# Kernel optimization log

Measured on AMD Instinct MI355X. Metric: run time of the kernel, lower is better.

The kernel has to match this reference:

```python
import jax, jax.numpy as jnp
import numpy as np

DIM = 1024
STATE = 256
B, S = 4, 4096

def setup_inputs() -> dict:
    key = jax.random.key(0)
    ks = jax.random.split(key, 8)
    sc_b = 1.0 / np.sqrt(DIM)
    sc_c = 1.0 / np.sqrt(STATE)
    return {
        "x": jax.random.normal(ks[0], (B, S, DIM), dtype=jnp.float32),
        "A": jax.random.normal(ks[1], (STATE,), dtype=jnp.float32) * 0.02,
        "B_w": jax.random.uniform(ks[2], (STATE, DIM), minval=-sc_b, maxval=sc_b),
        "B_b": jax.random.uniform(ks[3], (STATE,), minval=-sc_b, maxval=sc_b),
        "C_w": jax.random.uniform(ks[4], (DIM, STATE), minval=-sc_c, maxval=sc_c),
        "C_b": jax.random.uniform(ks[5], (DIM,), minval=-sc_c, maxval=sc_c),
        "D_w": jax.random.uniform(ks[6], (DIM, DIM), minval=-sc_b, maxval=sc_b),
        "D_b": jax.random.uniform(ks[7], (DIM,), minval=-sc_b, maxval=sc_b),
    }

def reference(x, A, B_w, B_b, C_w, C_b, D_w, D_b):
    # Precompute input projections in batch (the per-step loop only needs state*A + Bu)
    Bu = jnp.einsum('bsd,nd->bsn', x, B_w) + B_b          # [B,S,STATE]
    Du = jnp.einsum('bsd,ed->bse', x, D_w) + D_b          # [B,S,DIM]
    Aexp = jnp.exp(A)[None, :]                             # [1,STATE]
    state0 = jnp.zeros((x.shape[0], A.shape[0]), dtype=x.dtype)

    def step(state, bu_t):
        state = jnp.tanh(state * Aexp + bu_t)
        return state, state

    _, states = jax.lax.scan(step, state0, jnp.swapaxes(Bu, 0, 1))  # [S,B,STATE]
    states = jnp.swapaxes(states, 0, 1)                              # [B,S,STATE]
    y = jnp.einsum('bsn,en->bse', states, C_w) + C_b + Du
    return y
```

## Files before the change

kernel.cpp:

```cpp
#include <hip/hip_runtime.h>
#include <hip/hip_bf16.h>

#define DIM 1024
#define STATE 256
#define BATCH 4
#define SEQ 4096
#define M_TOT (BATCH * SEQ)

typedef short short8 __attribute__((ext_vector_type(8)));
typedef float f32x4 __attribute__((ext_vector_type(4)));

__device__ __forceinline__ unsigned short f2bf(float f) {
  unsigned int u = __float_as_uint(f);
  u += 0x7fff + ((u >> 16) & 1);
  return (unsigned short)(u >> 16);
}

__device__ __forceinline__ void gl_lds16(const void* g, void* l) {
  __builtin_amdgcn_global_load_lds(
      (const __attribute__((address_space(1))) void*)g,
      (__attribute__((address_space(3))) void*)l, 16, 0, 0);
}

#define C2F 2.8853900817779268f
#define LOG2EF 1.4426950408889634f

__global__ __launch_bounds__(256) void convert_kernel(
    const float* __restrict__ x, const float* __restrict__ A,
    const float* __restrict__ Bw, const float* __restrict__ Bb,
    const float* __restrict__ Cw, const float* __restrict__ Cb,
    const float* __restrict__ Dw, const float* __restrict__ Db,
    unsigned short* __restrict__ xb, unsigned short* __restrict__ bwb,
    unsigned short* __restrict__ wob, float* __restrict__ bb2,
    float* __restrict__ mP2, float* __restrict__ cbdb) {
  const int bx = blockIdx.x;
  const int t = threadIdx.x;
  if (bx < 16384) {
    size_t i = ((size_t)bx * 256 + t) * 4;
    const float4 v = *(const float4*)(x + i);
    *(ushort4*)(xb + i) = make_ushort4(f2bf(v.x), f2bf(v.y), f2bf(v.z), f2bf(v.w));
  } else if (bx < 16384 + 256) {
    int r = bx - 16384;
    int c = t * 4;
    const float4 v = *(const float4*)(Bw + (size_t)r * DIM + c);
    *(ushort4*)(bwb + (size_t)r * DIM + c) =
        make_ushort4(f2bf(v.x), f2bf(v.y), f2bf(v.z), f2bf(v.w));
  } else if (bx < 16384 + 256 + 1024) {
    int e = bx - 16384 - 256;
    if (t < 64) {
      const float4 v = *(const float4*)(Cw + (size_t)e * STATE + t * 4);
      *(ushort4*)(wob + (size_t)e * 1280 + t * 4) =
          make_ushort4(f2bf(v.x), f2bf(v.y), f2bf(v.z), f2bf(v.w));
    }
    const float4 v = *(const float4*)(Dw + (size_t)e * DIM + t * 4);
    *(ushort4*)(wob + (size_t)e * 1280 + 256 + t * 4) =
        make_ushort4(f2bf(v.x), f2bf(v.y), f2bf(v.z), f2bf(v.w));
  } else {
    const float P = C2F * __builtin_amdgcn_exp2f(A[t] * LOG2EF);
    bb2[t] = fmaf(Bb[t], C2F, P);
    mP2[t] = -2.0f * P;
#pragma unroll
    for (int k = 0; k < 4; ++k) {
      const int i = t * 4 + k;
      cbdb[i] = Cb[i] + Db[i];
    }
  }
}

__global__ __launch_bounds__(256, 2) void gemm_G(
    const unsigned short* __restrict__ A,
    const unsigned short* __restrict__ B,
    float* __restrict__ G,
    const float* __restrict__ bb2) {
  __shared__ unsigned short As[128 * 32];
  __shared__ unsigned short Bs[128 * 32];

  const int tid = threadIdx.x;
  const int wave = tid >> 6;
  const int lane = tid & 63;
  const int lr = lane & 15;
  const int lk = lane >> 4;
  const int wr = wave >> 1;
  const int wc = wave & 1;

  const int ntile = blockIdx.x & 1;
  const int mtile = blockIdx.x >> 1;
  const int m0 = mtile * 128;
  const int n0 = ntile * 128;

  f32x4 acc[4][4];
#pragma unroll
  for (int i = 0; i < 4; ++i)
#pragma unroll
    for (int j = 0; j < 4; ++j) acc[i][j] = (f32x4){0.f, 0.f, 0.f, 0.f};

  const char* Abyte = (const char*)A;
  const char* Bbyte = (const char*)B;
  char* AsB = (char*)As;
  char* BsB = (char*)Bs;

  for (int k0 = 0; k0 < 1024; k0 += 32) {
#pragma unroll
    for (int i = 0; i < 2; ++i) {
      const int o = i * 4096 + tid * 16;
      const int r = o >> 6;
      const int cb = o & 63;
      gl_lds16(Abyte + (size_t)(m0 + r) * 2048 + (size_t)k0 * 2 + cb,
               AsB + i * 4096 + wave * 1024);
      gl_lds16(Bbyte + (size_t)(n0 + r) * 2048 + (size_t)k0 * 2 + cb,
               BsB + i * 4096 + wave * 1024);
    }
    __syncthreads();

    short8 af[4], bfr[4];
#pragma unroll
    for (int f = 0; f < 4; ++f) {
      af[f]  = *(const short8*)(AsB + (wr * 64 + f * 16 + lr) * 64 + lk * 16);
      bfr[f] = *(const short8*)(BsB + (wc * 64 + f * 16 + lr) * 64 + lk * 16);
    }
#pragma unroll
    for (int i = 0; i < 4; ++i)
#pragma unroll
      for (int j = 0; j < 4; ++j)
        acc[i][j] = __builtin_amdgcn_mfma_f32_16x16x32_bf16(af[i], bfr[j], acc[i][j], 0, 0, 0);
    __syncthreads();
  }

#pragma unroll
  for (int fi = 0; fi < 4; ++fi)
#pragma unroll
    for (int fj = 0; fj < 4; ++fj)
#pragma unroll
      for (int j = 0; j < 4; ++j) {
        const int rg = m0 + wr * 64 + fi * 16 + lk * 4 + j;
        const int cg = n0 + wc * 64 + fj * 16 + lr;
        G[(size_t)rg * STATE + cg] = fmaf(acc[fi][fj][j], C2F, bb2[cg]);
      }
}

__global__ __launch_bounds__(256) void scan_kernel(
    const float* __restrict__ G, const float* __restrict__ mP2arr,
    unsigned short* __restrict__ states) {
  const int b = blockIdx.x >> 6;
  const int chunk = blockIdx.x & 63;
  const int n = threadIdx.x;
  const int t0 = chunk * 64;
  const int start = (t0 > 192) ? (t0 - 192) : 0;
  const int nw = t0 - start;
  const int total = nw + 64;

  const float* g = G + ((size_t)b * SEQ + start) * STATE + n;
  unsigned short* q = states + ((size_t)b * SEQ + start) * STATE + n;
  const float mP2 = mP2arr[n];

  float r = 0.5f;
  constexpr int CH = 16;
  float cur[CH], nxt[CH];
#pragma unroll
  for (int j = 0; j < CH; ++j) cur[j] = g[(size_t)j * STATE];

  const int NC = total / CH;
  for (int c = 0; c < NC; ++c) {
    if (c + 1 < NC) {
      const float* pn = g + (size_t)(c + 1) * CH * STATE;
#pragma unroll
      for (int j = 0; j < CH; ++j) nxt[j] = pn[(size_t)j * STATE];
    }
    if (c * CH >= nw) {
      unsigned short* qc = q + (size_t)c * CH * STATE;
#pragma unroll
      for (int j = 0; j < CH; ++j) {
        const float t = fmaf(mP2, r, cur[j]);
        const float e = __builtin_amdgcn_exp2f(t);
        r = __builtin_amdgcn_rcpf(1.0f + e);
        const float s = fmaf(-2.0f, r, 1.0f);
        qc[(size_t)j * STATE] = f2bf(s);
      }
    } else {
#pragma unroll
      for (int j = 0; j < CH; ++j) {
        const float t = fmaf(mP2, r, cur[j]);
        const float e = __builtin_amdgcn_exp2f(t);
        r = __builtin_amdgcn_rcpf(1.0f + e);
      }
    }
    if (c + 1 < NC) {
#pragma unroll
      for (int j = 0; j < CH; ++j) cur[j] = nxt[j];
    }
  }
}

#define VMC(N) asm volatile("s_waitcnt vmcnt(" #N ")" ::: "memory")

#define PH(TILE, Q, STG, VMST)                                                 \
  do {                                                                         \
    const char* As = lds + ((TILE) & 1) * 32768;                               \
    const char* Bs = lds + 65536 + ((TILE) & 1) * 32768;                       \
    if ((Q) == 0) {                                                            \
      _Pragma("unroll") for (int fj = 0; fj < 4; ++fj) {                       \
        const int r = wn * 64 + fj * 16 + lr;                                  \
        _Pragma("unroll") for (int kk = 0; kk < 2; ++kk)                       \
          bfr[fj][kk] = *(const short8*)(Bs + r * 128 +                        \
                                         (((kk * 4 + lk) ^ (r & 7)) << 4));    \
      }                                                                        \
    }                                                                          \
    short8 af[2][2];                                                           \
    _Pragma("unroll") for (int fl = 0; fl < 2; ++fl) {                         \
      const int r = wm * 128 + (Q) * 32 + fl * 16 + lr;                        \
      _Pragma("unroll") for (int kk = 0; kk < 2; ++kk)                         \
        af[fl][kk] = *(const short8*)(As + r * 128 +                           \
                                      (((kk * 4 + lk) ^ (r & 7)) << 4));       \
    }                                                                          \
    STG;                                                                       \
    __builtin_amdgcn_s_barrier();                                              \
    __builtin_amdgcn_s_setprio(1);                                             \
    _Pragma("unroll") for (int kk = 0; kk < 2; ++kk)                           \
      _Pragma("unroll") for (int fl = 0; fl < 2; ++fl)                         \
        _Pragma("unroll") for (int fj = 0; fj < 4; ++fj)                       \
          acc[(Q) * 2 + fl][fj] = __builtin_amdgcn_mfma_f32_16x16x32_bf16(     \
              af[fl][kk], bfr[fj][kk], acc[(Q) * 2 + fl][fj], 0, 0, 0);        \
    __builtin_amdgcn_s_setprio(0);                                             \
    VMST;                                                                      \
    __builtin_amdgcn_s_barrier();                                              \
  } while (0)

__global__ __launch_bounds__(512, 2) void gemm_out(
    const unsigned short* __restrict__ stb,
    const unsigned short* __restrict__ xb,
    const unsigned short* __restrict__ wob,
    const float* __restrict__ cbdb,
    float* __restrict__ dout)
{
  __shared__ char lds[131072];

  const int tid = threadIdx.x;
  const int wave = tid >> 6;
  const int lane = tid & 63;
  const int lr = lane & 15;
  const int lk = lane >> 4;
  const int wm = wave >> 2;
  const int wn = wave & 3;

  const int bs = ((blockIdx.x & 7) << 5) | (blockIdx.x >> 3);
  const int m0 = (bs >> 2) * 256;
  const int n0 = (bs & 3) * 256;

  const char* stbB = (const char*)stb;
  const char* xbB  = (const char*)xb;
  const char* wobB = (const char*)wob;

  f32x4 acc[8][4];
#pragma unroll
  for (int i = 0; i < 8; ++i)
#pragma unroll
    for (int j = 0; j < 4; ++j) acc[i][j] = (f32x4){0.f, 0.f, 0.f, 0.f};

  auto stageA = [&](int kt, int h) {
    if (kt >= 20) return;
    const char* base;
    size_t str;
    size_t colb;
    if (kt < 4) { base = stbB; str = 512;  colb = (size_t)kt * 128; }
    else        { base = xbB;  str = 2048; colb = (size_t)(kt - 4) * 128; }
    base += (size_t)m0 * str;
#pragma unroll
    for (int i2 = 0; i2 < 2; ++i2) {
      const int s = i2 * 512 + tid;
      const int r = s >> 3;
      const int cl = (s & 7) ^ (r & 7);
      gl_lds16(base + (size_t)(h * 128 + r) * str + colb + cl * 16,
               lds + ((kt & 1) * 32768) + h * 16384 + i2 * 8192 + wave * 1024);
    }
  };
  auto stageB = [&](int kt, int h) {
    if (kt >= 20) return;
#pragma unroll
    for (int i2 = 0; i2 < 2; ++i2) {
      const int s = i2 * 512 + tid;
      const int r = s >> 3;
      const int cl = (s & 7) ^ (r & 7);
      gl_lds16(wobB + (size_t)(n0 + h * 128 + r) * 2560 + (size_t)kt * 128 + cl * 16,
               lds + 65536 + ((kt & 1) * 32768) + h * 16384 + i2 * 8192 + wave * 1024);
    }
  };

  stageA(0, 0); stageA(0, 1);
  stageB(0, 0); stageB(0, 1);
  stageB(1, 0); stageB(1, 1);
  VMC(4);
  __builtin_amdgcn_s_barrier();

  short8 bfr[4][2];
  for (int i = 0; i < 10; ++i) {
    const int e = 2 * i, o = e + 1;
    PH(e, 0, stageA(o, 0), );
    PH(e, 1, stageA(o, 1), );
    PH(e, 2, stageB(e + 2, 0), );
    PH(e, 3, stageB(e + 2, 1), if (i == 9) { VMC(0); } else { VMC(4); });
    PH(o, 0, stageA(e + 2, 0), );
    PH(o, 1, stageA(e + 2, 1), );
    PH(o, 2, stageB(o + 2, 0), );
    PH(o, 3, stageB(o + 2, 1), VMC(4));
  }

#pragma unroll
  for (int fj = 0; fj < 4; ++fj) {
    const int col = n0 + wn * 64 + fj * 16 + lr;
    const float cb = cbdb[col];
#pragma unroll
    for (int m = 0; m < 8; ++m) {
      const int rowb = m0 + wm * 128 + m * 16 + lk * 4;
#pragma unroll
      for (int j = 0; j < 4; ++j)
        dout[(size_t)(rowb + j) * DIM + col] = acc[m][fj][j] + cb;
    }
  }
}

extern "C" void kernel_launch(void* const* d_in, const int* in_sizes, int n_in,
                              void* d_out, int out_size, void* d_ws, size_t ws_size,
                              hipStream_t stream) {
  const float* x  = (const float*)d_in[0];
  const float* A  = (const float*)d_in[1];
  const float* Bw = (const float*)d_in[2];
  const float* Bb = (const float*)d_in[3];
  const float* Cw = (const float*)d_in[4];
  const float* Cb = (const float*)d_in[5];
  const float* Dw = (const float*)d_in[6];
  const float* Db = (const float*)d_in[7];
  float* dout = (float*)d_out;

  char* ws = (char*)d_ws;
  unsigned short* xb   = (unsigned short*)(ws);
  unsigned short* bwb  = (unsigned short*)(ws + 33554432);
  unsigned short* wob  = (unsigned short*)(ws + 34078720);
  float*          G    = (float*)         (ws + 36700160);
  unsigned short* stb  = (unsigned short*)(ws + 53477376);
  float*          bb2  = (float*)         (ws + 61865984);
  float*          mP2  = (float*)         (ws + 61867008);
  float*          cbdb = (float*)         (ws + 61868032);

  convert_kernel<<<16384 + 256 + 1024 + 1, 256, 0, stream>>>(
      x, A, Bw, Bb, Cw, Cb, Dw, Db, xb, bwb, wob, bb2, mP2, cbdb);
  gemm_G<<<256, 256, 0, stream>>>(xb, bwb, G, bb2);
  scan_kernel<<<BATCH * 64, 256, 0, stream>>>(G, mP2, stb);
  gemm_out<<<256, 512, 0, stream>>>(stb, xb, wob, cbdb, dout);
}
```

Baseline: 102.5 us.

## Fuse x fp32-to-bf16 conversion into the Bu GEMM and shorten scan warmup

The separate conversion pass over x is removed. The first GEMM now loads fp32 x straight into swizzled LDS, converts it to bf16 in registers before the MFMAs, and the ntile==0 blocks write the bf16 copy of x back for the later output GEMM. This saves one full read and write pass over x and one kernel's worth of work, at the cost of more LDS per block and a different block-to-tile ordering. The scan warmup window drops from 192 to 128 steps, which trades some accuracy margin for less redundant work, and an lgkmcnt wait is added in the output GEMM phase macro.

```diff
diff --git a/kernel.cpp b/kernel.cpp
--- a/kernel.cpp
+++ b/kernel.cpp
@@ -24,29 +24,24 @@
 
 #define C2F 2.8853900817779268f
 #define LOG2EF 1.4426950408889634f
-
-__global__ __launch_bounds__(256) void convert_kernel(
-    const float* __restrict__ x, const float* __restrict__ A,
-    const float* __restrict__ Bw, const float* __restrict__ Bb,
-    const float* __restrict__ Cw, const float* __restrict__ Cb,
-    const float* __restrict__ Dw, const float* __restrict__ Db,
-    unsigned short* __restrict__ xb, unsigned short* __restrict__ bwb,
+#define VMC(N) asm volatile("s_waitcnt vmcnt(" #N ")" ::: "memory")
+
+__global__ __launch_bounds__(256) void convert_w(
+    const float* __restrict__ A, const float* __restrict__ Bw,
+    const float* __restrict__ Bb, const float* __restrict__ Cw,
+    const float* __restrict__ Cb, const float* __restrict__ Dw,
+    const float* __restrict__ Db, unsigned short* __restrict__ bwb,
     unsigned short* __restrict__ wob, float* __restrict__ bb2,
     float* __restrict__ mP2, float* __restrict__ cbdb) {
   const int bx = blockIdx.x;
   const int t = threadIdx.x;
-  if (bx < 16384) {
-    size_t i = ((size_t)bx * 256 + t) * 4;
-    const float4 v = *(const float4*)(x + i);
-    *(ushort4*)(xb + i) = make_ushort4(f2bf(v.x), f2bf(v.y), f2bf(v.z), f2bf(v.w));
-  } else if (bx < 16384 + 256) {
-    int r = bx - 16384;
+  if (bx < 256) {
     int c = t * 4;
-    const float4 v = *(const float4*)(Bw + (size_t)r * DIM + c);
-    *(ushort4*)(bwb + (size_t)r * DIM + c) =
+    const float4 v = *(const float4*)(Bw + (size_t)bx * DIM + c);
+    *(ushort4*)(bwb + (size_t)bx * DIM + c) =
         make_ushort4(f2bf(v.x), f2bf(v.y), f2bf(v.z), f2bf(v.w));
-  } else if (bx < 16384 + 256 + 1024) {
-    int e = bx - 16384 - 256;
+  } else if (bx < 256 + 1024) {
+    int e = bx - 256;
     if (t < 64) {
       const float4 v = *(const float4*)(Cw + (size_t)e * STATE + t * 4);
       *(ushort4*)(wob + (size_t)e * 1280 + t * 4) =
@@ -67,13 +62,15 @@
   }
 }
 
-__global__ __launch_bounds__(256, 2) void gemm_G(
-    const unsigned short* __restrict__ A,
-    const unsigned short* __restrict__ B,
+__global__ __launch_bounds__(256, 3) void gemm_GX(
+    const float* __restrict__ x,
+    const unsigned short* __restrict__ bwb,
     float* __restrict__ G,
-    const float* __restrict__ bb2) {
-  __shared__ unsigned short As[128 * 32];
-  __shared__ unsigned short Bs[128 * 32];
+    const float* __restrict__ bb2,
+    unsigned short* __restrict__ xb)
+{
+  __shared__ char AsB[32768];
+  __shared__ char BsB[16384];
 
   const int tid = threadIdx.x;
   const int wave = tid >> 6;
@@ -83,8 +80,9 @@
   const int wr = wave >> 1;
   const int wc = wave & 1;
 
-  const int ntile = blockIdx.x & 1;
-  const int mtile = blockIdx.x >> 1;
+  const int bs = (blockIdx.x & 7) * 32 + (blockIdx.x >> 3);
+  const int mtile = bs >> 1;
+  const int ntile = bs & 1;
   const int m0 = mtile * 128;
   const int n0 = ntile * 128;
 
@@ -94,35 +92,73 @@
 #pragma unroll
     for (int j = 0; j < 4; ++j) acc[i][j] = (f32x4){0.f, 0.f, 0.f, 0.f};
 
-  const char* Abyte = (const char*)A;
-  const char* Bbyte = (const char*)B;
-  char* AsB = (char*)As;
-  char* BsB = (char*)Bs;
-
-  for (int k0 = 0; k0 < 1024; k0 += 32) {
-#pragma unroll
-    for (int i = 0; i < 2; ++i) {
-      const int o = i * 4096 + tid * 16;
-      const int r = o >> 6;
-      const int cb = o & 63;
-      gl_lds16(Abyte + (size_t)(m0 + r) * 2048 + (size_t)k0 * 2 + cb,
+  const char* xB  = (const char*)x;
+  const char* bwB = (const char*)bwb;
+  char* xbB = (char*)xb;
+
+  for (int k0 = 0; k0 < 1024; k0 += 64) {
+#pragma unroll
+    for (int i = 0; i < 8; ++i) {
+      const int s = i * 256 + tid;
+      const int r = s >> 4;
+      const int c = (s & 15) ^ (r & 7);
+      gl_lds16(xB + (size_t)(m0 + r) * 4096 + (size_t)k0 * 4 + c * 16,
                AsB + i * 4096 + wave * 1024);
-      gl_lds16(Bbyte + (size_t)(n0 + r) * 2048 + (size_t)k0 * 2 + cb,
+    }
+#pragma unroll
+    for (int i = 0; i < 4; ++i) {
+      const int s = i * 256 + tid;
+      const int r = s >> 3;
+      const int c = (s & 7) ^ (r & 7);
+      gl_lds16(bwB + (size_t)(n0 + r) * 2048 + (size_t)k0 * 2 + c * 16,
                BsB + i * 4096 + wave * 1024);
     }
     __syncthreads();
 
-    short8 af[4], bfr[4];
-#pragma unroll
-    for (int f = 0; f < 4; ++f) {
-      af[f]  = *(const short8*)(AsB + (wr * 64 + f * 16 + lr) * 64 + lk * 16);
-      bfr[f] = *(const short8*)(BsB + (wc * 64 + f * 16 + lr) * 64 + lk * 16);
-    }
-#pragma unroll
-    for (int i = 0; i < 4; ++i)
-#pragma unroll
-      for (int j = 0; j < 4; ++j)
-        acc[i][j] = __builtin_amdgcn_mfma_f32_16x16x32_bf16(af[i], bfr[j], acc[i][j], 0, 0, 0);
+#pragma unroll
+    for (int kk = 0; kk < 2; ++kk) {
+      short8 af[4], bfr[4];
+#pragma unroll
+      for (int f = 0; f < 4; ++f) {
+        const int ra = wr * 64 + f * 16 + lr;
+        const int swa = ra & 7;
+        const f32x4 a0 = *(const f32x4*)(AsB + ra * 256 + (((kk * 8 + 2 * lk) ^ swa) << 4));
+        const f32x4 a1 = *(const f32x4*)(AsB + ra * 256 + (((kk * 8 + 2 * lk + 1) ^ swa) << 4));
+        short8 v;
+#pragma unroll
+        for (int j = 0; j < 4; ++j) {
+          v[j]     = (short)f2bf(a0[j]);
+          v[4 + j] = (short)f2bf(a1[j]);
+        }
+        af[f] = v;
+        const int rb = wc * 64 + f * 16 + lr;
+        bfr[f] = *(const short8*)(BsB + rb * 128 + (((kk * 4 + lk) ^ (rb & 7)) << 4));
+      }
+#pragma unroll
+      for (int i = 0; i < 4; ++i)
+#pragma unroll
+        for (int j = 0; j < 4; ++j)
+          acc[i][j] = __builtin_amdgcn_mfma_f32_16x16x32_bf16(af[i], bfr[j], acc[i][j], 0, 0, 0);
+    }
+
+    if (ntile == 0) {
+#pragma unroll
+      for (int i = 0; i < 4; ++i) {
+        const int o = i * 256 + tid;
+        const int r = o >> 3;
+        const int oc = o & 7;
+        const int sw = r & 7;
+        const f32x4 a0 = *(const f32x4*)(AsB + r * 256 + (((2 * oc) ^ sw) << 4));
+        const f32x4 a1 = *(const f32x4*)(AsB + r * 256 + (((2 * oc + 1) ^ sw) << 4));
+        short8 v;
+#pragma unroll
+        for (int j = 0; j < 4; ++j) {
+          v[j]     = (short)f2bf(a0[j]);
+          v[4 + j] = (short)f2bf(a1[j]);
+        }
+        *(short8*)(xbB + (size_t)(m0 + r) * 2048 + (size_t)k0 * 2 + oc * 16) = v;
+      }
+    }
     __syncthreads();
   }
 
@@ -145,7 +181,7 @@
   const int chunk = blockIdx.x & 63;
   const int n = threadIdx.x;
   const int t0 = chunk * 64;
-  const int start = (t0 > 192) ? (t0 - 192) : 0;
+  const int start = (t0 > 128) ? (t0 - 128) : 0;
   const int nw = t0 - start;
   const int total = nw + 64;
 
@@ -190,8 +226,6 @@
     }
   }
 }
-
-#define VMC(N) asm volatile("s_waitcnt vmcnt(" #N ")" ::: "memory")
 
 #define PH(TILE, Q, STG, VMST)                                                 \
   do {                                                                         \
@@ -213,6 +247,7 @@
                                       (((kk * 4 + lk) ^ (r & 7)) << 4));       \
     }                                                                          \
     STG;                                                                       \
+    if ((Q) == 0) asm volatile("s_waitcnt lgkmcnt(8)" ::: "memory");           \
     __builtin_amdgcn_s_barrier();                                              \
     __builtin_amdgcn_s_setprio(1);                                             \
     _Pragma("unroll") for (int kk = 0; kk < 2; ++kk)                           \
@@ -341,9 +376,9 @@
   float*          mP2  = (float*)         (ws + 61867008);
   float*          cbdb = (float*)         (ws + 61868032);
 
-  convert_kernel<<<16384 + 256 + 1024 + 1, 256, 0, stream>>>(
-      x, A, Bw, Bb, Cw, Cb, Dw, Db, xb, bwb, wob, bb2, mP2, cbdb);
-  gemm_G<<<256, 256, 0, stream>>>(xb, bwb, G, bb2);
+  convert_w<<<256 + 1024 + 1, 256, 0, stream>>>(
+      A, Bw, Bb, Cw, Cb, Dw, Db, bwb, wob, bb2, mP2, cbdb);
+  gemm_GX<<<256, 256, 0, stream>>>(x, bwb, G, bb2, xb);
   scan_kernel<<<BATCH * 64, 256, 0, stream>>>(G, mP2, stb);
   gemm_out<<<256, 512, 0, stream>>>(stb, xb, wob, cbdb, dout);
 }
```

New measurement: 100.6 us. No clear change (-1.8%).
